# Optimization experiments

Hardware: AMD Instinct MI355X
Metric: run time of the kernel (lower is better)

## Reference

```python
import jax, jax.numpy as jnp
import numpy as np

N_NODES = 100000
N_EDGES = 1600000
D = 128
NUM_GRAPHS = 128


def setup_inputs() -> dict:
    key = jax.random.key(0)
    ks = jax.random.split(key, 9)
    s = 1.0 / np.sqrt(D)
    return {
        "h": jax.random.normal(ks[0], (N_NODES, D), dtype=jnp.float32),
        "W1_self": jax.random.normal(ks[1], (D, D), dtype=jnp.float32) * s,
        "W1_neigh": jax.random.normal(ks[2], (D, D), dtype=jnp.float32) * s,
        "b1": jnp.zeros((D,), dtype=jnp.float32),
        "W2_self": jax.random.normal(ks[3], (D, D), dtype=jnp.float32) * s,
        "W2_neigh": jax.random.normal(ks[4], (D, D), dtype=jnp.float32) * s,
        "b2": jnp.zeros((D,), dtype=jnp.float32),
        "src": jax.random.randint(ks[5], (N_EDGES,), 0, N_NODES, dtype=jnp.int32),
        "dst": jax.random.randint(ks[6], (N_EDGES,), 0, N_NODES, dtype=jnp.int32),
        "graph_ids": jnp.sort(jax.random.randint(ks[7], (N_NODES,), 0, NUM_GRAPHS, dtype=jnp.int32)),
    }


def _sage_conv(h, src, dst, W_self, W_neigh, b, deg_inv):
    # mean-aggregate in-neighbor features: gather src feats, segment-sum by dst
    agg = jax.ops.segment_sum(h[src], dst, num_segments=h.shape[0])  # [N, D]
    h_neigh = agg * deg_inv[:, None]
    return h @ W_self + h_neigh @ W_neigh + b


def reference(h, W1_self, W1_neigh, b1, W2_self, W2_neigh, b2, src, dst, graph_ids):
    N = h.shape[0]
    deg = jax.ops.segment_sum(jnp.ones_like(dst, dtype=h.dtype), dst, num_segments=N)
    deg_inv = jnp.where(deg > 0, 1.0 / jnp.maximum(deg, 1.0), 0.0)
    h1 = jax.nn.relu(_sage_conv(h, src, dst, W1_self, W1_neigh, b1, deg_inv))
    h2 = jax.nn.relu(_sage_conv(h1, src, dst, W2_self, W2_neigh, b2, deg_inv))
    # dgl.mean_nodes: per-graph mean of node features
    gsum = jax.ops.segment_sum(h2, graph_ids, num_segments=NUM_GRAPHS)  # [G, D]
    gcnt = jax.ops.segment_sum(jnp.ones((N,), dtype=h.dtype), graph_ids, num_segments=NUM_GRAPHS)
    return gsum / jnp.maximum(gcnt, 1.0)[:, None]
```

## Files before the change

### kernel.cpp

```cpp
#include <hip/hip_runtime.h>

#define N_NODES   100000
#define N_EDGES   1600000
#define D         128
#define NUM_GRAPHS 128

#define NB          196
#define BUCKET_NODES 512
#define BUCKET_CAP  10240
#define EPB         8192

#define N_TILES32   3125
#define GEMM_BLOCKS 782

typedef __attribute__((ext_vector_type(8)))  short bf16x8;
typedef __attribute__((ext_vector_type(8)))  unsigned short u16x8;
typedef __attribute__((ext_vector_type(4)))  unsigned short u16x4;
typedef __attribute__((ext_vector_type(2)))  unsigned int u32x2;
typedef __attribute__((ext_vector_type(4)))  unsigned int u32x4;
typedef __attribute__((ext_vector_type(16))) float f32x16;

__device__ __forceinline__ float bf2f(unsigned short v) {
    return __uint_as_float(((unsigned int)v) << 16);
}
__device__ __forceinline__ unsigned short f2bf(float f) {
    unsigned int u = __float_as_uint(f);
    u = (u + 0x7FFFu + ((u >> 16) & 1u)) >> 16;
    return (unsigned short)u;
}

__device__ __forceinline__ void acc_f8(float* acc, u32x2 v) {
    auto a0 = __builtin_amdgcn_cvt_pk_f32_fp8((int)v[0], false);
    auto a1 = __builtin_amdgcn_cvt_pk_f32_fp8((int)v[0], true);
    auto a2 = __builtin_amdgcn_cvt_pk_f32_fp8((int)v[1], false);
    auto a3 = __builtin_amdgcn_cvt_pk_f32_fp8((int)v[1], true);
    acc[0] += a0[0]; acc[1] += a0[1]; acc[2] += a1[0]; acc[3] += a1[1];
    acc[4] += a2[0]; acc[5] += a2[1]; acc[6] += a3[0]; acc[7] += a3[1];
}

__device__ __forceinline__ bf16x8 f8_to_bf16x8(u32x2 v) {
    auto f0 = __builtin_amdgcn_cvt_pk_f32_fp8((int)v[0], false);
    auto f1 = __builtin_amdgcn_cvt_pk_f32_fp8((int)v[0], true);
    auto f2 = __builtin_amdgcn_cvt_pk_f32_fp8((int)v[1], false);
    auto f3 = __builtin_amdgcn_cvt_pk_f32_fp8((int)v[1], true);
    u16x8 p;
    p[0] = f2bf(f0[0]); p[1] = f2bf(f0[1]); p[2] = f2bf(f1[0]); p[3] = f2bf(f1[1]);
    p[4] = f2bf(f2[0]); p[5] = f2bf(f2[1]); p[6] = f2bf(f3[0]); p[7] = f2bf(f3[1]);
    return *(bf16x8*)&p;
}

__global__ void k_misc(u32x4* __restrict__ zp, int n16,
                       const int* __restrict__ gid, int* __restrict__ gcnt,
                       const float* __restrict__ W1s, const float* __restrict__ W1n,
                       unsigned short* __restrict__ Wt1,
                       const float* __restrict__ W2s, const float* __restrict__ W2n,
                       unsigned short* __restrict__ Wt2) {
    const int b = blockIdx.x;
    if (b < 17) {
        int i = b * 256 + threadIdx.x;
        if (i < n16) zp[i] = (u32x4){0u, 0u, 0u, 0u};
    } else if (b == 17) {
        int g = threadIdx.x;
        if (g >= NUM_GRAPHS) return;
        int lo = 0, hi = N_NODES;
        while (lo < hi) { int mid = (lo + hi) >> 1; if (gid[mid] < g) lo = mid + 1; else hi = mid; }
        int beg = lo;
        hi = N_NODES;
        while (lo < hi) { int mid = (lo + hi) >> 1; if (gid[mid] < g + 1) lo = mid + 1; else hi = mid; }
        gcnt[g] = lo - beg;
    } else if (b < 146) {
        int idx = (b - 18) * 256 + threadIdx.x;
        int j  = idx & 7;
        int l  = (idx >> 3) & 63;
        int fs = idx >> 9;
        int ct = fs >> 4, kt = fs & 15;
        int n  = ct * 32 + (l & 31);
        int k  = kt * 16 + 8 * (l >> 5) + j;
        float v = (k < 128) ? W1s[k * D + n] : W1n[(k - 128) * D + n];
        Wt1[idx] = f2bf(v);
    } else {
        int idx = (b - 146) * 256 + threadIdx.x;
        int j  = idx & 7;
        int l  = (idx >> 3) & 63;
        int fs = idx >> 9;
        int ct = fs >> 4, kt = fs & 15;
        int n  = ct * 32 + (l & 31);
        int k  = kt * 16 + 8 * (l >> 5) + j;
        int p  = k & 127;
        int c  = 32 * (p & 3) + (p >> 2);
        float v = (k < 128) ? W2s[c * D + n] : W2n[c * D + n];
        Wt2[idx] = f2bf(v);
    }
}

__global__ __launch_bounds__(256) void k_binplace(const int* __restrict__ src,
                                                  const int* __restrict__ dst,
                                                  int* __restrict__ gcur,
                                                  unsigned int* __restrict__ binned) {
    __shared__ unsigned int stag[EPB];
    __shared__ unsigned char sbk[EPB];
    __shared__ int hist[NB], lstart[NB], lcur[NB], gclaim[NB];
    __shared__ int scan[256];
    const int t = threadIdx.x;
    const int e0 = blockIdx.x * EPB;

    if (t < NB) hist[t] = 0;
    __syncthreads();

    int pk[32]; int bk[32];
#pragma unroll
    for (int i = 0; i < 32; ++i) {
        int e = e0 + t + 256 * i;
        if (e < N_EDGES) {
            int s = src[e], d = dst[e];
            bk[i] = d >> 9;
            pk[i] = (s << 9) | (d & 511);
            atomicAdd(&hist[bk[i]], 1);
        } else {
            bk[i] = -1; pk[i] = 0;
        }
    }
    __syncthreads();

    int hv = (t < NB) ? hist[t] : 0;
    scan[t] = hv;
    __syncthreads();
    for (int off = 1; off < 256; off <<= 1) {
        int add = (t >= off) ? scan[t - off] : 0;
        __syncthreads();
        scan[t] += add;
        __syncthreads();
    }
    if (t < NB) {
        int ex = scan[t] - hv;
        lstart[t] = ex;
        lcur[t]   = ex;
        gclaim[t] = atomicAdd(&gcur[t], hv);
    }
    __syncthreads();

#pragma unroll
    for (int i = 0; i < 32; ++i) {
        if (bk[i] >= 0) {
            int p = atomicAdd(&lcur[bk[i]], 1);
            stag[p] = (unsigned int)pk[i];
            sbk[p] = (unsigned char)bk[i];
        }
    }
    __syncthreads();

    const int total = scan[NB - 1];
    for (int j = t; j < total; j += 256) {
        int b = sbk[j];
        binned[(size_t)b * BUCKET_CAP + gclaim[b] + (j - lstart[b])] = stag[j];
    }
}

__global__ __launch_bounds__(256) void k_fill2(const unsigned int* __restrict__ binned,
                                               const int* __restrict__ gcur,
                                               int* __restrict__ adj,
                                               int* __restrict__ row_start,
                                               int* __restrict__ row_len) {
    __shared__ int hist[BUCKET_NODES], lstart[BUCKET_NODES], lcur[BUCKET_NODES];
    __shared__ int s2[256];
    const int t = threadIdx.x;
    const int b = blockIdx.x;
    const int C = gcur[b];
    const unsigned int* bp = binned + (size_t)b * BUCKET_CAP;

    hist[t] = 0; hist[t + 256] = 0;
    __syncthreads();
    for (int j = t; j < C; j += 256)
        atomicAdd(&hist[bp[j] & 511], 1);
    __syncthreads();

    int h0 = hist[2 * t], h1 = hist[2 * t + 1];
    int sv = h0 + h1;
    s2[t] = sv;
    __syncthreads();
    for (int off = 1; off < 256; off <<= 1) {
        int add = (t >= off) ? s2[t - off] : 0;
        __syncthreads();
        s2[t] += add;
        __syncthreads();
    }
    int ex = s2[t] - sv;
    lstart[2 * t] = ex;          lcur[2 * t] = ex;
    lstart[2 * t + 1] = ex + h0; lcur[2 * t + 1] = ex + h0;
    __syncthreads();

    for (int dl = t; dl < BUCKET_NODES; dl += 256) {
        int n = b * BUCKET_NODES + dl;
        if (n < N_NODES) {
            row_start[n] = b * BUCKET_CAP + lstart[dl];
            row_len[n]   = hist[dl];
        }
    }

    for (int j = t; j < C; j += 256) {
        unsigned int v = bp[j];
        int dl = v & 511;
        int pos = atomicAdd(&lcur[dl], 1);
        adj[(size_t)b * BUCKET_CAP + pos] = (int)(v >> 9);
    }
}

__global__ void k_cast_h(const float* __restrict__ h, unsigned char* __restrict__ h8) {
    int i = blockIdx.x * 256 + threadIdx.x;
    if (i >= N_NODES * (D / 8)) return;
    const float4* hv = (const float4*)h;
    float4 x = hv[2 * i], y = hv[2 * i + 1];
    int lo = __builtin_amdgcn_cvt_pk_fp8_f32(x.x, x.y, 0, false);
    lo = __builtin_amdgcn_cvt_pk_fp8_f32(x.z, x.w, lo, true);
    int hi = __builtin_amdgcn_cvt_pk_fp8_f32(y.x, y.y, 0, false);
    hi = __builtin_amdgcn_cvt_pk_fp8_f32(y.z, y.w, hi, true);
    u32x2 q; q[0] = (unsigned int)lo; q[1] = (unsigned int)hi;
    *(u32x2*)(h8 + (size_t)i * 8) = q;
}

__global__ __launch_bounds__(256) void k_agg_f8(const unsigned char* __restrict__ hin,
                                                const int* __restrict__ row_start,
                                                const int* __restrict__ row_len,
                                                const int* __restrict__ adj,
                                                unsigned short* __restrict__ hout) {
    int node = blockIdx.x * 16 + (threadIdx.x >> 4);
    int sub = threadIdx.x & 15;
    if (node >= N_NODES) return;
    int beg = row_start[node];
    int len = row_len[node];
    int end = beg + len;
    const unsigned char* hsub = hin + sub * 8;
    float acc[8];
#pragma unroll
    for (int i = 0; i < 8; ++i) acc[i] = 0.f;
    int j = beg;
    for (; j + 7 < end; j += 8) {
        u32x2 v0 = *(const u32x2*)(hsub + (size_t)adj[j]     * D);
        u32x2 v1 = *(const u32x2*)(hsub + (size_t)adj[j + 1] * D);
        u32x2 v2 = *(const u32x2*)(hsub + (size_t)adj[j + 2] * D);
        u32x2 v3 = *(const u32x2*)(hsub + (size_t)adj[j + 3] * D);
        u32x2 v4 = *(const u32x2*)(hsub + (size_t)adj[j + 4] * D);
        u32x2 v5 = *(const u32x2*)(hsub + (size_t)adj[j + 5] * D);
        u32x2 v6 = *(const u32x2*)(hsub + (size_t)adj[j + 6] * D);
        u32x2 v7 = *(const u32x2*)(hsub + (size_t)adj[j + 7] * D);
        acc_f8(acc, v0); acc_f8(acc, v1); acc_f8(acc, v2); acc_f8(acc, v3);
        acc_f8(acc, v4); acc_f8(acc, v5); acc_f8(acc, v6); acc_f8(acc, v7);
    }
    for (; j + 3 < end; j += 4) {
        u32x2 v0 = *(const u32x2*)(hsub + (size_t)adj[j]     * D);
        u32x2 v1 = *(const u32x2*)(hsub + (size_t)adj[j + 1] * D);
        u32x2 v2 = *(const u32x2*)(hsub + (size_t)adj[j + 2] * D);
        u32x2 v3 = *(const u32x2*)(hsub + (size_t)adj[j + 3] * D);
        acc_f8(acc, v0); acc_f8(acc, v1); acc_f8(acc, v2); acc_f8(acc, v3);
    }
    for (; j < end; ++j) {
        u32x2 v0 = *(const u32x2*)(hsub + (size_t)adj[j] * D);
        acc_f8(acc, v0);
    }
    float inv = (len > 0) ? 1.f / (float)len : 0.f;
    u16x8 p;
#pragma unroll
    for (int i = 0; i < 8; ++i) p[i] = f2bf(acc[i] * inv);
    *(u16x8*)(hout + (size_t)node * D + sub * 8) = p;
}

template <int POOL>
__global__ __launch_bounds__(256) void k_gemm_mfma(
    const unsigned char* __restrict__ X0, const unsigned short* __restrict__ X1,
    const unsigned short* __restrict__ Wtp, const float* __restrict__ bias,
    unsigned char* __restrict__ outp8,
    const int* __restrict__ gid, float* __restrict__ gsum) {
    __shared__ unsigned short WS[D * 256];
    const int tid = threadIdx.x;
    const int wave = tid >> 6, lane = tid & 63;
    const int l31 = lane & 31, half = lane >> 5;
    const int gw = blockIdx.x * 4 + wave;
    const bool act = (gw < N_TILES32);

    bf16x8 a[16];
    if (act) {
        const int row = gw * 32 + l31;
        const unsigned char*  x0 = X0 + (size_t)row * D + half * 8;
        const unsigned short* x1 = X1 + (size_t)row * D + half * 8;
        u32x2 v8[8];
#pragma unroll
        for (int kt = 0; kt < 8; ++kt)
            v8[kt] = *(const u32x2*)(x0 + kt * 16);
#pragma unroll
        for (int kt = 0; kt < 8; ++kt)
            a[8 + kt] = *(const bf16x8*)(x1 + kt * 16);
#pragma unroll
        for (int kt = 0; kt < 8; ++kt)
            a[kt] = f8_to_bf16x8(v8[kt]);
    }

    {
        const u16x8* g = (const u16x8*)Wtp;
        u16x8* s = (u16x8*)WS;
#pragma unroll
        for (int i = 0; i < 16; ++i) s[i * 256 + tid] = g[i * 256 + tid];
    }
    __syncthreads();
    if (!act) return;

    f32x16 acc[4];
#pragma unroll
    for (int ct = 0; ct < 4; ++ct)
#pragma unroll
        for (int i = 0; i < 16; ++i) acc[ct][i] = 0.f;

#pragma unroll
    for (int cp = 0; cp < 2; ++cp) {
        const int c0 = 2 * cp, c1 = 2 * cp + 1;
#pragma unroll
        for (int kt = 0; kt < 16; ++kt) {
            bf16x8 b0 = *(const bf16x8*)&WS[((c0 * 16 + kt) * 64 + lane) * 8];
            bf16x8 b1 = *(const bf16x8*)&WS[((c1 * 16 + kt) * 64 + lane) * 8];
            acc[c0] = __builtin_amdgcn_mfma_f32_32x32x16_bf16(a[kt], b0, acc[c0], 0, 0, 0);
            acc[c1] = __builtin_amdgcn_mfma_f32_32x32x16_bf16(a[kt], b1, acc[c1], 0, 0, 0);
        }
    }

    const int trow0 = gw * 32;
    float bia[4];
#pragma unroll
    for (int ct = 0; ct < 4; ++ct) bia[ct] = bias[ct * 32 + l31];

    if (POOL == 0) {
#pragma unroll
        for (int r = 0; r < 16; ++r) {
            int row = trow0 + (r & 3) + 8 * (r >> 2) + 4 * half;
            float f[4];
#pragma unroll
            for (int ct = 0; ct < 4; ++ct)
                f[ct] = fmaxf(acc[ct][r] + bia[ct], 0.f);
            int p8 = __builtin_amdgcn_cvt_pk_fp8_f32(f[0], f[1], 0, false);
            p8 = __builtin_amdgcn_cvt_pk_fp8_f32(f[2], f[3], p8, true);
            *(unsigned int*)(outp8 + (size_t)row * D + l31 * 4) = (unsigned int)p8;
        }
    } else {
        int g[16];
#pragma unroll
        for (int r = 0; r < 16; ++r)
            g[r] = gid[trow0 + (r & 3) + 8 * (r >> 2) + 4 * half];
#pragma unroll
        for (int ct = 0; ct < 4; ++ct) {
            int c = ct * 32 + l31;
            float run = 0.f; int curg = -1;
#pragma unroll
            for (int r = 0; r < 16; ++r) {
                float v = fmaxf(acc[ct][r] + bia[ct], 0.f);
                if (g[r] != curg) {
                    if (curg >= 0) atomicAdd(&gsum[curg * D + c], run);
                    curg = g[r]; run = v;
                } else {
                    run += v;
                }
            }
            if (curg >= 0) atomicAdd(&gsum[curg * D + c], run);
        }
    }
}

__global__ void k_final(const float* __restrict__ gsum, const int* __restrict__ gcnt,
                        float* __restrict__ out) {
    int i = blockIdx.x * blockDim.x + threadIdx.x;
    if (i < NUM_GRAPHS * D) {
        int g = i >> 7;
        int c = gcnt[g];
        out[i] = gsum[i] / (float)(c > 0 ? c : 1);
    }
}

extern "C" void kernel_launch(void* const* d_in, const int* in_sizes, int n_in,
                              void* d_out, int out_size, void* d_ws, size_t ws_size,
                              hipStream_t stream) {
    const float* h   = (const float*)d_in[0];
    const float* W1s = (const float*)d_in[1];
    const float* W1n = (const float*)d_in[2];
    const float* b1  = (const float*)d_in[3];
    const float* W2s = (const float*)d_in[4];
    const float* W2n = (const float*)d_in[5];
    const float* b2  = (const float*)d_in[6];
    const int* src   = (const int*)d_in[7];
    const int* dst   = (const int*)d_in[8];
    const int* gids  = (const int*)d_in[9];
    float* out = (float*)d_out;
    char* ws = (char*)d_ws;

    size_t off = 0;
    auto alloc = [&](size_t bytes) {
        size_t o = off;
        off = (off + bytes + 255) & ~(size_t)255;
        return o;
    };
    size_t z0         = off;
    size_t gcur_off   = alloc((size_t)NB * 4);
    size_t gsum_off   = alloc((size_t)NUM_GRAPHS * D * 4);
    size_t zlen       = off - z0;
    size_t gcnt_off   = alloc((size_t)NUM_GRAPHS * 4);
    size_t rs_off     = alloc((size_t)N_NODES * 4);
    size_t rl_off     = alloc((size_t)N_NODES * 4);
    size_t bin_off    = alloc((size_t)NB * BUCKET_CAP * 4);
    size_t adj_off    = alloc((size_t)NB * BUCKET_CAP * 4);
    size_t hn_off     = alloc((size_t)N_NODES * D * 2);
    size_t h8_off     = alloc((size_t)N_NODES * D);
    size_t h18_off    = alloc((size_t)N_NODES * D);
    size_t wt1_off    = alloc((size_t)D * 256 * 2);
    size_t wt2_off    = alloc((size_t)D * 256 * 2);
    (void)ws_size;

    int*   gcur      = (int*)(ws + gcur_off);
    int*   gcnt      = (int*)(ws + gcnt_off);
    float* gsum      = (float*)(ws + gsum_off);
    int*   row_start = (int*)(ws + rs_off);
    int*   row_len   = (int*)(ws + rl_off);
    unsigned int* binned = (unsigned int*)(ws + bin_off);
    int*   adj       = (int*)(ws + adj_off);
    unsigned short* hn  = (unsigned short*)(ws + hn_off);
    unsigned char*  h8   = (unsigned char*)(ws + h8_off);
    unsigned char*  h1p8 = (unsigned char*)(ws + h18_off);
    unsigned short* Wt1 = (unsigned short*)(ws + wt1_off);
    unsigned short* Wt2 = (unsigned short*)(ws + wt2_off);

    const int n16 = (int)(zlen / 16);

    k_misc<<<274, 256, 0, stream>>>((u32x4*)(ws + z0), n16, gids, gcnt,
                                    W1s, W1n, Wt1, W2s, W2n, Wt2);

    const int nbin_blocks = (N_EDGES + EPB - 1) / EPB;
    k_binplace<<<nbin_blocks, 256, 0, stream>>>(src, dst, gcur, binned);
    k_fill2<<<NB, 256, 0, stream>>>(binned, gcur, adj, row_start, row_len);

    k_cast_h<<<(N_NODES * (D / 8) + 255) / 256, 256, 0, stream>>>(h, h8);

    const int agg_blocks = (N_NODES + 15) / 16;

    k_agg_f8<<<agg_blocks, 256, 0, stream>>>(h8, row_start, row_len, adj, hn);
    k_gemm_mfma<0><<<GEMM_BLOCKS, 256, 0, stream>>>(h8, hn, Wt1, b1, h1p8,
                                                    nullptr, nullptr);
    k_agg_f8<<<agg_blocks, 256, 0, stream>>>(h1p8, row_start, row_len, adj, hn);
    k_gemm_mfma<1><<<GEMM_BLOCKS, 256, 0, stream>>>(h1p8, hn, Wt2, b2, nullptr,
                                                    gids, gsum);

    k_final<<<(NUM_GRAPHS * D + 255) / 256, 256, 0, stream>>>(gsum, gcnt, out);
}
```

Measured before the change: 173.0 us.

## Store aggregated neighbor features as fp8 and fuse h cast into setup kernel

The neighbor-mean output of the aggregation kernel is now stored as fp8 instead of bf16, which halves its write traffic and the GEMM's read of that operand. The GEMM converts both operands from fp8 to bf16. The fp8-to-bf16 conversion now truncates with a byte permute instead of rounding, which is exact because fp8 values fit in bf16. The standalone h-to-fp8 cast kernel is folded into the misc setup kernel to save one launch. The cost is extra quantisation error on the aggregated features.

```diff
diff --git a/kernel.cpp b/kernel.cpp
--- a/kernel.cpp
+++ b/kernel.cpp
@@ -15,14 +15,10 @@
 
 typedef __attribute__((ext_vector_type(8)))  short bf16x8;
 typedef __attribute__((ext_vector_type(8)))  unsigned short u16x8;
-typedef __attribute__((ext_vector_type(4)))  unsigned short u16x4;
 typedef __attribute__((ext_vector_type(2)))  unsigned int u32x2;
 typedef __attribute__((ext_vector_type(4)))  unsigned int u32x4;
 typedef __attribute__((ext_vector_type(16))) float f32x16;
 
-__device__ __forceinline__ float bf2f(unsigned short v) {
-    return __uint_as_float(((unsigned int)v) << 16);
-}
 __device__ __forceinline__ unsigned short f2bf(float f) {
     unsigned int u = __float_as_uint(f);
     u = (u + 0x7FFFu + ((u >> 16) & 1u)) >> 16;
@@ -43,10 +39,12 @@
     auto f1 = __builtin_amdgcn_cvt_pk_f32_fp8((int)v[0], true);
     auto f2 = __builtin_amdgcn_cvt_pk_f32_fp8((int)v[1], false);
     auto f3 = __builtin_amdgcn_cvt_pk_f32_fp8((int)v[1], true);
-    u16x8 p;
-    p[0] = f2bf(f0[0]); p[1] = f2bf(f0[1]); p[2] = f2bf(f1[0]); p[3] = f2bf(f1[1]);
-    p[4] = f2bf(f2[0]); p[5] = f2bf(f2[1]); p[6] = f2bf(f3[0]); p[7] = f2bf(f3[1]);
-    return *(bf16x8*)&p;
+    u32x4 w;
+    w[0] = __builtin_amdgcn_perm(__float_as_uint(f0[1]), __float_as_uint(f0[0]), 0x07060302u);
+    w[1] = __builtin_amdgcn_perm(__float_as_uint(f1[1]), __float_as_uint(f1[0]), 0x07060302u);
+    w[2] = __builtin_amdgcn_perm(__float_as_uint(f2[1]), __float_as_uint(f2[0]), 0x07060302u);
+    w[3] = __builtin_amdgcn_perm(__float_as_uint(f3[1]), __float_as_uint(f3[0]), 0x07060302u);
+    return *(bf16x8*)&w;
 }
 
 __global__ void k_misc(u32x4* __restrict__ zp, int n16,
@@ -54,7 +52,8 @@
                        const float* __restrict__ W1s, const float* __restrict__ W1n,
                        unsigned short* __restrict__ Wt1,
                        const float* __restrict__ W2s, const float* __restrict__ W2n,
-                       unsigned short* __restrict__ Wt2) {
+                       unsigned short* __restrict__ Wt2,
+                       const float* __restrict__ h, unsigned char* __restrict__ h8) {
     const int b = blockIdx.x;
     if (b < 17) {
         int i = b * 256 + threadIdx.x;
@@ -78,7 +77,7 @@
         int k  = kt * 16 + 8 * (l >> 5) + j;
         float v = (k < 128) ? W1s[k * D + n] : W1n[(k - 128) * D + n];
         Wt1[idx] = f2bf(v);
-    } else {
+    } else if (b < 274) {
         int idx = (b - 146) * 256 + threadIdx.x;
         int j  = idx & 7;
         int l  = (idx >> 3) & 63;
@@ -90,6 +89,17 @@
         int c  = 32 * (p & 3) + (p >> 2);
         float v = (k < 128) ? W2s[c * D + n] : W2n[c * D + n];
         Wt2[idx] = f2bf(v);
+    } else {
+        int i = (b - 274) * 256 + threadIdx.x;
+        if (i >= N_NODES * (D / 8)) return;
+        const float4* hv = (const float4*)h;
+        float4 x = hv[2 * i], y = hv[2 * i + 1];
+        int lo = __builtin_amdgcn_cvt_pk_fp8_f32(x.x, x.y, 0, false);
+        lo = __builtin_amdgcn_cvt_pk_fp8_f32(x.z, x.w, lo, true);
+        int hi = __builtin_amdgcn_cvt_pk_fp8_f32(y.x, y.y, 0, false);
+        hi = __builtin_amdgcn_cvt_pk_fp8_f32(y.z, y.w, hi, true);
+        u32x2 q; q[0] = (unsigned int)lo; q[1] = (unsigned int)hi;
+        *(u32x2*)(h8 + (size_t)i * 8) = q;
     }
 }
 
@@ -205,24 +215,11 @@
     }
 }
 
-__global__ void k_cast_h(const float* __restrict__ h, unsigned char* __restrict__ h8) {
-    int i = blockIdx.x * 256 + threadIdx.x;
-    if (i >= N_NODES * (D / 8)) return;
-    const float4* hv = (const float4*)h;
-    float4 x = hv[2 * i], y = hv[2 * i + 1];
-    int lo = __builtin_amdgcn_cvt_pk_fp8_f32(x.x, x.y, 0, false);
-    lo = __builtin_amdgcn_cvt_pk_fp8_f32(x.z, x.w, lo, true);
-    int hi = __builtin_amdgcn_cvt_pk_fp8_f32(y.x, y.y, 0, false);
-    hi = __builtin_amdgcn_cvt_pk_fp8_f32(y.z, y.w, hi, true);
-    u32x2 q; q[0] = (unsigned int)lo; q[1] = (unsigned int)hi;
-    *(u32x2*)(h8 + (size_t)i * 8) = q;
-}
-
 __global__ __launch_bounds__(256) void k_agg_f8(const unsigned char* __restrict__ hin,
                                                 const int* __restrict__ row_start,
                                                 const int* __restrict__ row_len,
                                                 const int* __restrict__ adj,
-                                                unsigned short* __restrict__ hout) {
+                                                unsigned char* __restrict__ hout) {
     int node = blockIdx.x * 16 + (threadIdx.x >> 4);
     int sub = threadIdx.x & 15;
     if (node >= N_NODES) return;
@@ -258,15 +255,17 @@
         acc_f8(acc, v0);
     }
     float inv = (len > 0) ? 1.f / (float)len : 0.f;
-    u16x8 p;
-#pragma unroll
-    for (int i = 0; i < 8; ++i) p[i] = f2bf(acc[i] * inv);
-    *(u16x8*)(hout + (size_t)node * D + sub * 8) = p;
+    int lo = __builtin_amdgcn_cvt_pk_fp8_f32(acc[0] * inv, acc[1] * inv, 0, false);
+    lo = __builtin_amdgcn_cvt_pk_fp8_f32(acc[2] * inv, acc[3] * inv, lo, true);
+    int hi = __builtin_amdgcn_cvt_pk_fp8_f32(acc[4] * inv, acc[5] * inv, 0, false);
+    hi = __builtin_amdgcn_cvt_pk_fp8_f32(acc[6] * inv, acc[7] * inv, hi, true);
+    u32x2 q; q[0] = (unsigned int)lo; q[1] = (unsigned int)hi;
+    *(u32x2*)(hout + (size_t)node * D + sub * 8) = q;
 }
 
 template <int POOL>
 __global__ __launch_bounds__(256) void k_gemm_mfma(
-    const unsigned char* __restrict__ X0, const unsigned short* __restrict__ X1,
+    const unsigned char* __restrict__ X0, const unsigned char* __restrict__ X1,
     const unsigned short* __restrict__ Wtp, const float* __restrict__ bias,
     unsigned char* __restrict__ outp8,
     const int* __restrict__ gid, float* __restrict__ gsum) {
@@ -280,17 +279,17 @@
     bf16x8 a[16];
     if (act) {
         const int row = gw * 32 + l31;
-        const unsigned char*  x0 = X0 + (size_t)row * D + half * 8;
-        const unsigned short* x1 = X1 + (size_t)row * D + half * 8;
-        u32x2 v8[8];
+        const unsigned char* x0 = X0 + (size_t)row * D + half * 8;
+        const unsigned char* x1 = X1 + (size_t)row * D + half * 8;
+        u32x2 v8[16];
 #pragma unroll
         for (int kt = 0; kt < 8; ++kt)
             v8[kt] = *(const u32x2*)(x0 + kt * 16);
 #pragma unroll
         for (int kt = 0; kt < 8; ++kt)
-            a[8 + kt] = *(const bf16x8*)(x1 + kt * 16);
-#pragma unroll
-        for (int kt = 0; kt < 8; ++kt)
+            v8[8 + kt] = *(const u32x2*)(x1 + kt * 16);
+#pragma unroll
+        for (int kt = 0; kt < 16; ++kt)
             a[kt] = f8_to_bf16x8(v8[kt]);
     }
 
@@ -403,7 +402,7 @@
     size_t rl_off     = alloc((size_t)N_NODES * 4);
     size_t bin_off    = alloc((size_t)NB * BUCKET_CAP * 4);
     size_t adj_off    = alloc((size_t)NB * BUCKET_CAP * 4);
-    size_t hn_off     = alloc((size_t)N_NODES * D * 2);
+    size_t hn_off     = alloc((size_t)N_NODES * D);
     size_t h8_off     = alloc((size_t)N_NODES * D);
     size_t h18_off    = alloc((size_t)N_NODES * D);
     size_t wt1_off    = alloc((size_t)D * 256 * 2);
@@ -417,7 +416,7 @@
     int*   row_len   = (int*)(ws + rl_off);
     unsigned int* binned = (unsigned int*)(ws + bin_off);
     int*   adj       = (int*)(ws + adj_off);
-    unsigned short* hn  = (unsigned short*)(ws + hn_off);
+    unsigned char*  hn8  = (unsigned char*)(ws + hn_off);
     unsigned char*  h8   = (unsigned char*)(ws + h8_off);
     unsigned char*  h1p8 = (unsigned char*)(ws + h18_off);
     unsigned short* Wt1 = (unsigned short*)(ws + wt1_off);
@@ -425,22 +424,20 @@
 
     const int n16 = (int)(zlen / 16);
 
-    k_misc<<<274, 256, 0, stream>>>((u32x4*)(ws + z0), n16, gids, gcnt,
-                                    W1s, W1n, Wt1, W2s, W2n, Wt2);
+    k_misc<<<6524, 256, 0, stream>>>((u32x4*)(ws + z0), n16, gids, gcnt,
+                                     W1s, W1n, Wt1, W2s, W2n, Wt2, h, h8);
 
     const int nbin_blocks = (N_EDGES + EPB - 1) / EPB;
     k_binplace<<<nbin_blocks, 256, 0, stream>>>(src, dst, gcur, binned);
     k_fill2<<<NB, 256, 0, stream>>>(binned, gcur, adj, row_start, row_len);
 
-    k_cast_h<<<(N_NODES * (D / 8) + 255) / 256, 256, 0, stream>>>(h, h8);
-
     const int agg_blocks = (N_NODES + 15) / 16;
 
-    k_agg_f8<<<agg_blocks, 256, 0, stream>>>(h8, row_start, row_len, adj, hn);
-    k_gemm_mfma<0><<<GEMM_BLOCKS, 256, 0, stream>>>(h8, hn, Wt1, b1, h1p8,
+    k_agg_f8<<<agg_blocks, 256, 0, stream>>>(h8, row_start, row_len, adj, hn8);
+    k_gemm_mfma<0><<<GEMM_BLOCKS, 256, 0, stream>>>(h8, hn8, Wt1, b1, h1p8,
                                                     nullptr, nullptr);
-    k_agg_f8<<<agg_blocks, 256, 0, stream>>>(h1p8, row_start, row_len, adj, hn);
-    k_gemm_mfma<1><<<GEMM_BLOCKS, 256, 0, stream>>>(h1p8, hn, Wt2, b2, nullptr,
+    k_agg_f8<<<agg_blocks, 256, 0, stream>>>(h1p8, row_start, row_len, adj, hn8);
+    k_gemm_mfma<1><<<GEMM_BLOCKS, 256, 0, stream>>>(h1p8, hn8, Wt2, b2, nullptr,
                                                     gids, gsum);
 
     k_final<<<(NUM_GRAPHS * D + 255) / 256, 256, 0, stream>>>(gsum, gcnt, out);
```

After: 167.7 us. 1.03x faster.
